# Performance work log

Hardware: AMD Instinct MI355X
Metric: run time of the kernel (lower is better)

The kernel has to match this reference:

```python
import jax, jax.numpy as jnp
import numpy as np

B, T, D = 1, 2048, 4096
N, K, H = 32, 8, 128  # num_heads, num_kv_heads, head_dim
ROPE_BASE = 10000
SCALE_FACTOR = 1.0
EPS = 1e-6
NEG_INF = -1e9


def rms_norm(x):
    var = jnp.mean(jnp.square(x), axis=-1, keepdims=True)
    return x * jax.lax.rsqrt(var + EPS)


def apply_rope(x, positions, base_frequency, scale_factor=1.0):
    # x: [B, L, num_heads, H], positions: [B, L]
    head_dim = x.shape[-1]
    fraction = 2.0 * jnp.arange(head_dim // 2, dtype=jnp.float32) / head_dim
    timescale = base_frequency ** fraction  # [H/2]
    sinusoid = positions[..., None].astype(jnp.float32) / timescale  # [B,L,H/2]
    sinusoid = sinusoid[..., None, :] / scale_factor  # [B,L,1,H/2]
    sin, cos = jnp.sin(sinusoid), jnp.cos(sinusoid)
    x1, x2 = jnp.split(x, 2, axis=-1)
    return jnp.concatenate([x1 * cos - x2 * sin, x2 * cos + x1 * sin], axis=-1)


def setup_inputs() -> dict:
    key = jax.random.key(0)
    ks = jax.random.split(key, 7)
    x = jax.random.normal(ks[0], (B, T, D), dtype=jnp.float32)
    segment_pos = jnp.broadcast_to(jnp.arange(T, dtype=jnp.int32)[None, :], (B, T))
    causal = jnp.tril(jnp.ones((T, T), dtype=bool))
    attn_mask = jnp.where(causal, 0.0, NEG_INF).astype(jnp.float32)[None]  # [B,T,S]
    attn_mask = jnp.broadcast_to(attn_mask, (B, T, T))
    q_w = jax.random.normal(ks[1], (N, D, H), dtype=jnp.float32) * (D ** -0.5)
    kv_w = jax.random.normal(ks[2], (2, K, D, H), dtype=jnp.float32) * (D ** -0.5)
    o_w = jax.random.normal(ks[3], (N, H, D), dtype=jnp.float32) * ((N * H) ** -0.5)
    q_scale = jax.random.normal(ks[4], (H,), dtype=jnp.float32) * 0.02  # RMSNorm scale (zeros-init style)
    k_scale = jax.random.normal(ks[5], (H,), dtype=jnp.float32) * 0.02
    return {"x": x, "segment_pos": segment_pos, "attn_mask": attn_mask,
            "q_w": q_w, "kv_w": kv_w, "o_w": o_w,
            "q_scale": q_scale, "k_scale": k_scale}


def reference(x, segment_pos, attn_mask, q_w, kv_w, o_w, q_scale, k_scale):
    # Projections
    q = jnp.einsum('BTD,NDH->BTNH', x, q_w)          # [B,T,N,H]
    kv = jnp.einsum('BSD,CKDH->CBSKH', x, kv_w)      # [2,B,S,K,H]
    k, v = kv[0], kv[1]
    # QK RMSNorm (with scale, (1+scale) convention) and value RMSNorm (no scale)
    q = rms_norm(q) * (1.0 + q_scale)
    k = rms_norm(k) * (1.0 + k_scale)
    v = rms_norm(v)
    # RoPE (standard path: positions are [B,L])
    q = apply_rope(q, segment_pos, ROPE_BASE, SCALE_FACTOR)
    k = apply_rope(k, segment_pos, ROPE_BASE, SCALE_FACTOR)
    # GQA grouping: [B,T,K,G,H]
    G = N // K
    qg = q.reshape(B, T, K, G, H)
    attn_logits = jnp.einsum('btkgh,bskh->bkgts', qg, k)  # [B,K,G,T,S]
    attn_logits = attn_logits + attn_mask[:, None, None, :, :]
    attn_weights = jax.nn.softmax(attn_logits, axis=-1).astype(v.dtype)
    out = jnp.einsum('bkgts,bskh->btkgh', attn_weights, v)  # [B,T,K,G,H]
    out = out.reshape(B, T, N, H)
    return jnp.einsum('BTNH,NHD->BTD', out, o_w)
```

## Files before the change

### kernel.cpp

```cpp
#include <hip/hip_runtime.h>
#include <stdint.h>


typedef __bf16 bf16x8 __attribute__((ext_vector_type(8)));
typedef float  f32x4  __attribute__((ext_vector_type(4)));

__device__ __forceinline__ uint16_t f2bf(float f) {
    union { float f; uint32_t u; } v; v.f = f;
    uint32_t r = v.u + 0x7fffu + ((v.u >> 16) & 1u);
    return (uint16_t)(r >> 16);
}

__device__ __forceinline__ void gload_lds16(const void* g, void* l) {
    __builtin_amdgcn_global_load_lds(
        (const __attribute__((address_space(1))) uint32_t*)g,
        (__attribute__((address_space(3))) uint32_t*)l, 16, 0, 0);
}

__global__ __launch_bounds__(256) void k_cvt_x(const float* __restrict__ x,
                                               uint16_t* __restrict__ xb) {
    int i = (blockIdx.x * 256 + threadIdx.x) * 8;
    int r = i >> 12, k = i & 4095;
    float4 a = *(const float4*)(x + i);
    float4 b = *(const float4*)(x + i + 4);
    uint16_t tmp[8];
    tmp[0] = f2bf(a.x); tmp[1] = f2bf(a.y); tmp[2] = f2bf(a.z); tmp[3] = f2bf(a.w);
    tmp[4] = f2bf(b.x); tmp[5] = f2bf(b.y); tmp[6] = f2bf(b.z); tmp[7] = f2bf(b.w);
    int dst = r * 4096 + (k & ~63) + (((((k >> 3) & 7) ^ (r & 7))) << 3);
    *(uint4*)(xb + dst) = *(uint4*)tmp;
}

__global__ __launch_bounds__(256) void k_prep_wt(const float* __restrict__ qw,
                                                 const float* __restrict__ kvw,
                                                 uint16_t* __restrict__ Wt) {
    const int hx = blockIdx.x, dx = blockIdx.y, m = blockIdx.z;
    const float* src = (m < 32) ? (qw + (size_t)m * 524288)
                                : (kvw + (size_t)(m - 32) * 524288);
    __shared__ uint16_t tile[64][65];
    const int t = threadIdx.x, d0 = dx * 64, h0 = hx * 64;
#pragma unroll
    for (int i = 0; i < 16; ++i) {
        int idx = i * 256 + t, r = idx >> 6, c = idx & 63;
        tile[r][c] = f2bf(src[(size_t)(d0 + r) * 128 + h0 + c]);
    }
    __syncthreads();
#pragma unroll
    for (int it = 0; it < 2; ++it) {
        int slot = it * 256 + t, hr = slot >> 3, cl = slot & 7;
        int R = m * 128 + h0 + hr;
        uint16_t tmp[8];
#pragma unroll
        for (int e = 0; e < 8; ++e) tmp[e] = tile[cl * 8 + e][hr];
        *(uint4*)&Wt[(size_t)R * 4096 + d0 + ((cl ^ (R & 7)) << 3)] = *(uint4*)tmp;
    }
}

__global__ __launch_bounds__(256) void k_prep_ot(const float* __restrict__ ow,
                                                 uint16_t* __restrict__ Ot) {
    const int dx = blockIdx.x, hx = blockIdx.y, n = blockIdx.z;
    const float* src = ow + (size_t)n * 524288;
    __shared__ uint16_t tile[64][65];
    const int t = threadIdx.x, h0 = hx * 64, d0 = dx * 64;
#pragma unroll
    for (int i = 0; i < 16; ++i) {
        int idx = i * 256 + t, r = idx >> 6, c = idx & 63;
        tile[r][c] = f2bf(src[(size_t)(h0 + r) * 4096 + d0 + c]);
    }
    __syncthreads();
#pragma unroll
    for (int it = 0; it < 2; ++it) {
        int slot = it * 256 + t, dr = slot >> 3, cl = slot & 7;
        int R = d0 + dr;
        uint16_t tmp[8];
#pragma unroll
        for (int e = 0; e < 8; ++e) tmp[e] = tile[cl * 8 + e][dr];
        *(uint4*)&Ot[(size_t)R * 4096 + n * 128 + h0 + ((cl ^ (R & 7)) << 3)] = *(uint4*)tmp;
    }
}

#define PH_BAR do { asm volatile("" ::: "memory"); \
                    __builtin_amdgcn_s_barrier(); \
                    asm volatile("" ::: "memory"); } while (0)
#define WAIT_LGKM do { asm volatile("s_waitcnt lgkmcnt(0)" ::: "memory"); \
                       __builtin_amdgcn_sched_barrier(0); } while (0)
#define WAIT_VM(N) do { asm volatile("s_waitcnt vmcnt(" #N ")" ::: "memory"); \
                        __builtin_amdgcn_sched_barrier(0); } while (0)

__global__ __launch_bounds__(512, 2) void k_gemm_qkv(const uint16_t* __restrict__ A,
                                                     const uint16_t* __restrict__ Bt,
                                                     const int* __restrict__ pos,
                                                     const float* __restrict__ qs,
                                                     const float* __restrict__ ks,
                                                     uint16_t* __restrict__ Qg,
                                                     uint16_t* __restrict__ Kg,
                                                     uint16_t* __restrict__ Vg) {
    extern __shared__ __align__(16) char smem[];
    uint16_t* lds = (uint16_t*)smem;
    const int Kd = 4096;
    const int t = threadIdx.x, wid = t >> 6, lane = t & 63;
    const int l16 = lane & 15, quad = lane >> 4;
    const int wr = wid >> 2, wc = wid & 3;
    const int bx = blockIdx.x, bm0 = blockIdx.y * 256, bn0 = bx * 256;

    f32x4 acc[8][4];
    const f32x4 z4 = {0.f, 0.f, 0.f, 0.f};
#pragma unroll
    for (int i = 0; i < 8; ++i)
#pragma unroll
        for (int j = 0; j < 4; ++j) acc[i][j] = z4;

    const int r0 = wid * 16 + (lane >> 2), c4 = lane & 3;
    const int sw2 = (r0 >> 1) & 3, sw7 = r0 & 7;
    const int offK0 = (((c4 ^ sw2)) ^ sw7) * 8;
    const int offK1 = ((4 + (c4 ^ sw2)) ^ sw7) * 8;
    const uint16_t* pA0 = A + (size_t)(bm0 + r0) * Kd;
    const uint16_t* pA1 = pA0 + (size_t)128 * Kd;
    const uint16_t* pB0 = Bt + (size_t)(bn0 + r0) * Kd;
    const uint16_t* pB1 = pB0 + (size_t)128 * Kd;
    uint16_t* stA = lds + wid * 512;
    uint16_t* stB = lds + 32768 + wid * 512;

    const int sA = (l16 >> 1) & 3;
    const int rdA = (wr * 128 + l16) * 32 + ((quad ^ sA) << 3);
    const int rdB = 32768 + (wc * 64 + l16) * 32 + ((quad ^ sA) << 3);

    bf16x8 af[4], bf[4];

#define STAGE_A(SLAB, OFF, TT) do { \
    gload_lds16(pA0 + (size_t)(TT) * 64 + (OFF), stA + (SLAB) * 8192); \
    gload_lds16(pA1 + (size_t)(TT) * 64 + (OFF), stA + (SLAB) * 8192 + 4096); } while (0)
#define STAGE_B(SLAB, OFF, TT) do { \
    gload_lds16(pB0 + (size_t)(TT) * 64 + (OFF), stB + (SLAB) * 8192); \
    gload_lds16(pB1 + (size_t)(TT) * 64 + (OFF), stB + (SLAB) * 8192 + 4096); } while (0)
#define LOAD_AF4(SLAB, I0) do { _Pragma("unroll") \
    for (int i_ = 0; i_ < 4; ++i_) \
        af[i_] = *(const bf16x8*)&lds[(SLAB) * 8192 + rdA + ((I0) + i_) * 512]; } while (0)
#define LOAD_BF4(SLAB) do { _Pragma("unroll") \
    for (int j_ = 0; j_ < 4; ++j_) \
        bf[j_] = *(const bf16x8*)&lds[(SLAB) * 8192 + rdB + j_ * 512]; } while (0)
#define MFMA_PH(I0) do { __builtin_amdgcn_s_setprio(1); \
    _Pragma("unroll") for (int i_ = 0; i_ < 4; ++i_) \
        _Pragma("unroll") for (int j_ = 0; j_ < 4; ++j_) \
            acc[(I0) + i_][j_] = __builtin_amdgcn_mfma_f32_16x16x32_bf16(af[i_], bf[j_], acc[(I0) + i_][j_], 0, 0, 0); \
    __builtin_amdgcn_s_setprio(0); } while (0)

#define TILE(TT, BUF) do { \
     \
    LOAD_BF4(2*(BUF)); LOAD_AF4(2*(BUF), 0); \
    STAGE_A((((BUF)^1)*2+1), offK1, (TT)+1); \
    PH_BAR; WAIT_LGKM; MFMA_PH(0); PH_BAR; \
     \
    LOAD_AF4(2*(BUF), 4); \
    WAIT_VM(6); \
    STAGE_B((((BUF)^1)*2+1), offK1, (TT)+1); \
    PH_BAR; WAIT_LGKM; MFMA_PH(4); PH_BAR; \
     \
    LOAD_BF4(2*(BUF)+1); LOAD_AF4(2*(BUF)+1, 0); \
    STAGE_A((BUF)*2, offK0, (TT)+2); \
    PH_BAR; WAIT_LGKM; MFMA_PH(0); PH_BAR; \
     \
    LOAD_AF4(2*(BUF)+1, 4); \
    WAIT_VM(6); \
    STAGE_B((BUF)*2, offK0, (TT)+2); \
    PH_BAR; WAIT_LGKM; MFMA_PH(4); PH_BAR; \
} while (0)

    STAGE_A(0, offK0, 0); STAGE_B(0, offK0, 0);
    STAGE_A(1, offK1, 0); STAGE_B(1, offK1, 0);
    STAGE_A(2, offK0, 1); STAGE_B(2, offK0, 1);
    WAIT_VM(8);
    PH_BAR;

#pragma unroll 1
    for (int Ti = 0; Ti < 31; ++Ti) {
        TILE(2 * Ti, 0);
        TILE(2 * Ti + 1, 1);
    }

    STAGE_A(3, offK1, 63); STAGE_B(3, offK1, 63);
    WAIT_VM(0);
    PH_BAR;
#pragma unroll
    for (int T = 62; T < 64; ++T) {
        const int BUF = T & 1;
        LOAD_BF4(2*BUF); LOAD_AF4(2*BUF, 0);     PH_BAR; WAIT_LGKM; MFMA_PH(0); PH_BAR;
        LOAD_AF4(2*BUF, 4);                      PH_BAR; WAIT_LGKM; MFMA_PH(4); PH_BAR;
        LOAD_BF4(2*BUF+1); LOAD_AF4(2*BUF+1, 0); PH_BAR; WAIT_LGKM; MFMA_PH(0); PH_BAR;
        LOAD_AF4(2*BUF+1, 4);                    PH_BAR; WAIT_LGKM; MFMA_PH(4); PH_BAR;
    }

#undef TILE
#undef MFMA_PH
#undef LOAD_BF4
#undef LOAD_AF4
#undef STAGE_B
#undef STAGE_A

    float* X   = (float*)smem;
    float* ssq = (float*)(smem + 133120);

#pragma unroll
    for (int i = 0; i < 8; ++i)
#pragma unroll
        for (int r = 0; r < 4; ++r) {
            float s = 0.f;
#pragma unroll
            for (int j = 0; j < 4; ++j) s += acc[i][j][r] * acc[i][j][r];
            s += __shfl_xor(s, 1); s += __shfl_xor(s, 2);
            s += __shfl_xor(s, 4); s += __shfl_xor(s, 8);
            if (l16 == 0)
                ssq[(wr * 128 + i * 16 + quad * 4 + r) * 4 + (wc >> 1) * 2 + (wc & 1)] = s;
        }
    __syncthreads();

    const int cat = (bx < 16) ? 0 : (bx < 20 ? 1 : 2);
    float s1 = 0.f, s2 = 0.f, invts = 0.f;
    if (cat < 2) {
        const float* sc = cat ? ks : qs;
        s1 = 1.0f + sc[lane];
        s2 = 1.0f + sc[lane + 64];
        invts = exp2f((float)lane * -0.20762050593046014f);
    }

#pragma unroll
    for (int pass = 0; pass < 2; ++pass) {
        if (wr == pass) {
#pragma unroll
            for (int i = 0; i < 8; ++i)
#pragma unroll
                for (int j = 0; j < 4; ++j)
#pragma unroll
                    for (int r = 0; r < 4; ++r)
                        X[(i * 16 + quad * 4 + r) * 260 + wc * 64 + j * 16 + l16] = acc[i][j][r];
        }
        __syncthreads();
        for (int rr = 0; rr < 16; ++rr) {
            const int lrow = wid * 16 + rr;
            const int grow = bm0 + pass * 128 + lrow;
            float sn = 0.f, cs = 0.f;
            if (cat < 2) {
                float ang = (float)pos[grow] * invts;
                __sincosf(ang, &sn, &cs);
            }
#pragma unroll
            for (int hh = 0; hh < 2; ++hh) {
                const int sb = (pass * 128 + lrow) * 4 + hh * 2;
                float rn = rsqrtf((ssq[sb] + ssq[sb + 1]) * 0.0078125f + 1e-6f);
                float x1 = X[lrow * 260 + hh * 128 + lane];
                float x2 = X[lrow * 260 + hh * 128 + 64 + lane];
                if (cat < 2) {
                    float y1 = x1 * rn * s1, y2 = x2 * rn * s2;
                    X[lrow * 260 + hh * 128 + lane]      = y1 * cs - y2 * sn;
                    X[lrow * 260 + hh * 128 + 64 + lane] = y2 * cs + y1 * sn;
                } else {
                    X[lrow * 260 + hh * 128 + lane]      = x1 * rn;
                    X[lrow * 260 + hh * 128 + 64 + lane] = x2 * rn;
                }
            }
        }
        __syncthreads();
        if (cat == 2) {
#pragma unroll
            for (int it = 0; it < 8; ++it) {
                int slot = it * 512 + t, hh = slot >> 11, rem = slot & 2047;
                int h = rem >> 4, sc2 = rem & 15;
                uint16_t tmp[8];
#pragma unroll
                for (int e = 0; e < 8; ++e)
                    tmp[e] = f2bf(X[(sc2 * 8 + e) * 260 + hh * 128 + h]);
                int n = bx * 2 + hh;
                *(uint4*)&Vg[((size_t)(n - 40) * 128 + h) * 2048 + (bm0 + pass * 128)
                             + ((sc2 ^ (h & 15)) << 3)] = *(uint4*)tmp;
            }
        } else {
#pragma unroll
            for (int it = 0; it < 8; ++it) {
                int slot = it * 512 + t, hh = slot >> 11, rem = slot & 2047;
                int lrow = rem >> 4, c = rem & 15;
                int tg = bm0 + pass * 128 + lrow, n = bx * 2 + hh;
                f32x4 a = *(f32x4*)&X[lrow * 260 + hh * 128 + c * 8];
                f32x4 b = *(f32x4*)&X[lrow * 260 + hh * 128 + c * 8 + 4];
                uint16_t tmp[8];
#pragma unroll
                for (int e = 0; e < 4; ++e) { tmp[e] = f2bf(a[e]); tmp[4 + e] = f2bf(b[e]); }
                if (cat == 0)
                    *(uint4*)&Qg[((size_t)n * 2048 + tg) * 128 + c * 8] = *(uint4*)tmp;
                else
                    *(uint4*)&Kg[((size_t)(n - 32) * 2048 + tg) * 128
                                 + ((c ^ (tg & 15)) << 3)] = *(uint4*)tmp;
            }
        }
        __syncthreads();
    }
}

__global__ __launch_bounds__(512, 2) void k_gemm2p(const uint16_t* __restrict__ A,
                                                   const uint16_t* __restrict__ Bt,
                                                   float* __restrict__ C) {
    extern __shared__ __align__(16) char smem2[];
    uint16_t* lds = (uint16_t*)smem2;
    const int Kd = 4096, Nn = 4096;
    const int t = threadIdx.x, wid = t >> 6, lane = t & 63;
    const int l16 = lane & 15, quad = lane >> 4;
    const int wr = wid >> 1, wc = wid & 1;
    const int bm0 = blockIdx.y * 256, bn0 = blockIdx.x * 128;

    f32x4 acc[4][4];
    const f32x4 z4 = {0.f, 0.f, 0.f, 0.f};
#pragma unroll
    for (int i = 0; i < 4; ++i)
#pragma unroll
        for (int j = 0; j < 4; ++j) acc[i][j] = z4;

    const int r0 = wid * 16 + (lane >> 2), c4 = lane & 3;
    const int sw2 = (r0 >> 1) & 3, sw7 = r0 & 7;
    const int offK0 = ((c4 ^ sw2) ^ sw7) * 8;
    const int offK1 = ((4 + (c4 ^ sw2)) ^ sw7) * 8;
    const uint16_t* pA0 = A + (size_t)(bm0 + r0) * Kd;
    const uint16_t* pA1 = pA0 + (size_t)128 * Kd;
    const uint16_t* pB0 = Bt + (size_t)(bn0 + r0) * Kd;
    uint16_t* stA = lds + wid * 512;
    uint16_t* stB = lds + 49152 + wid * 512;

    const int sA = (l16 >> 1) & 3;
    const int rdA = (wr * 64 + l16) * 32 + ((quad ^ sA) << 3);
    const int rdB = 49152 + (wc * 64 + l16) * 32 + ((quad ^ sA) << 3);

    bf16x8 af[4], bf[4];

#define G2_STAGE(SLAB, OFF, TT) do { \
    gload_lds16(pA0 + (size_t)(TT) * 64 + (OFF), stA + (SLAB) * 8192); \
    gload_lds16(pA1 + (size_t)(TT) * 64 + (OFF), stA + (SLAB) * 8192 + 4096); \
    gload_lds16(pB0 + (size_t)(TT) * 64 + (OFF), stB + (SLAB) * 4096); } while (0)

#define G2_MFMA do { __builtin_amdgcn_s_setprio(1); \
    _Pragma("unroll") for (int i_ = 0; i_ < 4; ++i_) \
        _Pragma("unroll") for (int j_ = 0; j_ < 4; ++j_) \
            acc[i_][j_] = __builtin_amdgcn_mfma_f32_16x16x32_bf16(af[i_], bf[j_], acc[i_][j_], 0, 0, 0); \
    __builtin_amdgcn_s_setprio(0); } while (0)

#define G2_LOAD(CS) do { _Pragma("unroll") \
    for (int i_ = 0; i_ < 4; ++i_) \
        af[i_] = *(const bf16x8*)&lds[(CS) * 8192 + rdA + i_ * 512]; \
    _Pragma("unroll") for (int j_ = 0; j_ < 4; ++j_) \
        bf[j_] = *(const bf16x8*)&lds[(CS) * 4096 + rdB + j_ * 512]; } while (0)

#define G2_PH(CS, SG, OFF, TT) do { \
    G2_LOAD(CS); \
    WAIT_VM(6); \
    G2_STAGE((SG), (OFF), (TT)); \
    PH_BAR; WAIT_LGKM; G2_MFMA; PH_BAR; } while (0)

#define G2_PHT(CS, VMN) do { \
    G2_LOAD(CS); \
    WAIT_VM(VMN); \
    PH_BAR; WAIT_LGKM; G2_MFMA; PH_BAR; } while (0)

    G2_STAGE(0, offK0, 0);
    G2_STAGE(1, offK1, 0);
    G2_STAGE(2, offK0, 1);
    G2_STAGE(3, offK1, 1);
    WAIT_VM(9);
    PH_BAR;

#pragma unroll 1
    for (int Tb = 0; Tb < 60; Tb += 3) {
        G2_PH(0, 4, offK0, Tb + 2);  G2_PH(1, 5, offK1, Tb + 2);
        G2_PH(2, 0, offK0, Tb + 3);  G2_PH(3, 1, offK1, Tb + 3);
        G2_PH(4, 2, offK0, Tb + 4);  G2_PH(5, 3, offK1, Tb + 4);
    }
    G2_PH(0, 4, offK0, 62);  G2_PH(1, 5, offK1, 62);
    G2_PH(2, 0, offK0, 63);  G2_PH(3, 1, offK1, 63);
    G2_PHT(4, 6); G2_PHT(5, 3); G2_PHT(0, 0); G2_PHT(1, 0);

#undef G2_PHT
#undef G2_PH
#undef G2_LOAD
#undef G2_MFMA
#undef G2_STAGE

#pragma unroll
    for (int i = 0; i < 4; ++i)
#pragma unroll
        for (int j = 0; j < 4; ++j) {
            int row = bm0 + wr * 64 + i * 16 + quad * 4;
            int col = bn0 + wc * 64 + j * 16 + l16;
            float* cp = C + (size_t)row * Nn + col;
            cp[0]              = acc[i][j][0];
            cp[(size_t)Nn]     = acc[i][j][1];
            cp[2 * (size_t)Nn] = acc[i][j][2];
            cp[3 * (size_t)Nn] = acc[i][j][3];
        }
}

__global__ __launch_bounds__(256) void k_attn(const uint16_t* __restrict__ Q,
                                              const uint16_t* __restrict__ K,
                                              const uint16_t* __restrict__ Vt,
                                              uint16_t* __restrict__ att) {
    __shared__ uint16_t sK[128 * 128];
    __shared__ uint16_t sV[128 * 128];
    const int p = blockIdx.x, n = blockIdx.y, kk = n >> 2;
    const int t = threadIdx.x, wave = t >> 6, lane = t & 63;
    const int l16 = lane & 15, quad = lane >> 4;
    const f32x4 z4 = {0.f, 0.f, 0.f, 0.f};

    const uint16_t* Kbase = K  + ((size_t)kk * 2048 + wave * 32 + (lane >> 4)) * 128 + (lane & 15) * 8;
    const uint16_t* Vbase = Vt + ((size_t)kk * 128  + wave * 32 + (lane >> 4)) * 2048 + (lane & 15) * 8;

    for (int half = 0; half < 2; ++half) {
        const int qt = half ? (31 - p) : p;
        const int q0 = qt * 64;
        const int nk = (qt >> 1) + 1;

        bf16x8 qf[4];
#pragma unroll
        for (int kc = 0; kc < 4; ++kc)
            qf[kc] = *(const bf16x8*)(Q + (size_t)(n * 2048 + q0 + wave * 16 + l16) * 128 + kc * 32 + quad * 8);

        f32x4 O[8];
#pragma unroll
        for (int h = 0; h < 8; ++h) O[h] = z4;
        float mrow[4], lrow[4];
#pragma unroll
        for (int r = 0; r < 4; ++r) { mrow[r] = -INFINITY; lrow[r] = 0.f; }

        for (int st = 0; st < nk; ++st) {
            const int s0 = st * 128;
            __syncthreads();
#pragma unroll
            for (int j = 0; j < 8; ++j) {
                gload_lds16(Kbase + (size_t)(s0 + j * 4) * 128, &sK[(wave * 32 + j * 4) * 128]);
                gload_lds16(Vbase + (size_t)j * 4 * 2048 + s0,  &sV[(wave * 32 + j * 4) * 128]);
            }
            __syncthreads();

            f32x4 S[8];
#pragma unroll
            for (int jn = 0; jn < 8; ++jn) S[jn] = z4;
#pragma unroll
            for (int jn = 0; jn < 8; ++jn) {
                int krow = jn * 16 + l16;
#pragma unroll
                for (int kc = 0; kc < 4; ++kc) {
                    bf16x8 b = *(const bf16x8*)&sK[krow * 128 + (((kc * 4 + quad) ^ l16) << 3)];
                    S[jn] = __builtin_amdgcn_mfma_f32_16x16x32_bf16(qf[kc], b, S[jn], 0, 0, 0);
                }
            }
            if (st == nk - 1) {
#pragma unroll
                for (int jn = 0; jn < 8; ++jn) {
                    int sc = s0 + jn * 16 + l16;
#pragma unroll
                    for (int r = 0; r < 4; ++r) {
                        int mr = q0 + wave * 16 + quad * 4 + r;
                        if (sc > mr) S[jn][r] = -INFINITY;
                    }
                }
            }
            float alpha[4];
#pragma unroll
            for (int r = 0; r < 4; ++r) {
                float mx = S[0][r];
#pragma unroll
                for (int jn = 1; jn < 8; ++jn) mx = fmaxf(mx, S[jn][r]);
                mx = fmaxf(mx, __shfl_xor(mx, 1));
                mx = fmaxf(mx, __shfl_xor(mx, 2));
                mx = fmaxf(mx, __shfl_xor(mx, 4));
                mx = fmaxf(mx, __shfl_xor(mx, 8));
                float mnew = fmaxf(mrow[r], mx);
                float a = __expf(mrow[r] - mnew);
                mrow[r] = mnew;
                float sum = 0.f;
#pragma unroll
                for (int jn = 0; jn < 8; ++jn) {
                    float e = __expf(S[jn][r] - mnew);
                    S[jn][r] = e;
                    sum += e;
                }
                sum += __shfl_xor(sum, 1);
                sum += __shfl_xor(sum, 2);
                sum += __shfl_xor(sum, 4);
                sum += __shfl_xor(sum, 8);
                lrow[r] = lrow[r] * a + sum;
                alpha[r] = a;
            }
#pragma unroll
            for (int h = 0; h < 8; ++h)
#pragma unroll
                for (int r = 0; r < 4; ++r) O[h][r] *= alpha[r];

            __syncthreads();
#pragma unroll
            for (int jn = 0; jn < 8; ++jn)
#pragma unroll
                for (int r = 0; r < 4; ++r) {
                    int prow = wave * 16 + quad * 4 + r;
                    int pcol = jn * 16 + l16;
                    sK[prow * 128 + ((pcol & 7) | ((((pcol >> 3) ^ prow) & 15) << 3))]
                        = f2bf(S[jn][r]);
                }
            bf16x8 pf[4];
#pragma unroll
            for (int ksv = 0; ksv < 4; ++ksv)
                pf[ksv] = *(const bf16x8*)&sK[(wave * 16 + l16) * 128 + (((ksv * 4 + quad) ^ l16) << 3)];
#pragma unroll
            for (int hj = 0; hj < 8; ++hj) {
                int vrow = hj * 16 + l16;
#pragma unroll
                for (int ksv = 0; ksv < 4; ++ksv) {
                    bf16x8 b = *(const bf16x8*)&sV[vrow * 128 + (((ksv * 4 + quad) ^ l16) << 3)];
                    O[hj] = __builtin_amdgcn_mfma_f32_16x16x32_bf16(pf[ksv], b, O[hj], 0, 0, 0);
                }
            }
        }

        __syncthreads();
        uint16_t* sO = &sK[wave * 2112];
        float inv[4];
#pragma unroll
        for (int r = 0; r < 4; ++r) inv[r] = 1.0f / lrow[r];
#pragma unroll
        for (int hj = 0; hj < 8; ++hj)
#pragma unroll
            for (int r = 0; r < 4; ++r)
                sO[(quad * 4 + r) * 132 + hj * 16 + l16] = f2bf(O[hj][r] * inv[r]);
#pragma unroll
        for (int it = 0; it < 4; ++it) {
            int slot = it * 64 + lane, rloc = slot >> 4, cl = slot & 15;
            bf16x8 v = *(const bf16x8*)&sO[rloc * 132 + cl * 8];
            int R = q0 + wave * 16 + rloc;
            size_t dst = (size_t)R * 4096 + n * 128 + ((cl & 8) << 3) + (((cl & 7) ^ (R & 7)) << 3);
            *(uint4*)&att[dst] = *(uint4*)&v;
        }
    }
}

extern "C" void kernel_launch(void* const* d_in, const int* in_sizes, int n_in,
                              void* d_out, int out_size, void* d_ws, size_t ws_size,
                              hipStream_t stream) {
    const float* x   = (const float*)d_in[0];
    const int*   sp  = (const int*)d_in[1];
    const float* qw  = (const float*)d_in[3];
    const float* kvw = (const float*)d_in[4];
    const float* ow  = (const float*)d_in[5];
    const float* qsc = (const float*)d_in[6];
    const float* ksc = (const float*)d_in[7];
    float* out = (float*)d_out;

    char* ws = (char*)d_ws;
    uint16_t* xb   = (uint16_t*)(ws);
    uint16_t* Wt   = (uint16_t*)(ws + (size_t)(16u << 20));
    uint16_t* Qb   = (uint16_t*)(ws + (size_t)(64u << 20));
    uint16_t* Kb   = (uint16_t*)(ws + (size_t)(80u << 20));
    uint16_t* Vtb  = (uint16_t*)(ws + (size_t)(84u << 20));
    uint16_t* att  = (uint16_t*)(ws);
    uint16_t* Ot   = (uint16_t*)(ws + (size_t)(16u << 20));

    static bool attr_done = false;
    if (!attr_done) {
        hipFuncSetAttribute(reinterpret_cast<const void*>(k_gemm_qkv),
                            hipFuncAttributeMaxDynamicSharedMemorySize, 137216);
        hipFuncSetAttribute(reinterpret_cast<const void*>(k_gemm2p),
                            hipFuncAttributeMaxDynamicSharedMemorySize, 147456);
        attr_done = true;
    }

    k_cvt_x    <<<4096, 256, 0, stream>>>(x, xb);
    k_prep_wt  <<<dim3(2, 64, 48), 256, 0, stream>>>(qw, kvw, Wt);
    k_gemm_qkv <<<dim3(24, 8), 512, 137216, stream>>>(xb, Wt, sp, qsc, ksc, Qb, Kb, Vtb);
    k_prep_ot  <<<dim3(64, 2, 32), 256, 0, stream>>>(ow, Ot);
    k_attn     <<<dim3(16, 32), 256, 0, stream>>>(Qb, Kb, Vtb, att);
    k_gemm2p   <<<dim3(32, 8), 512, 147456, stream>>>(att, Ot, out);
}
```

Baseline: 530.6 us.

## Double-buffer MFMA operand registers to overlap LDS reads with MFMA in both GEMMs

Both GEMM main loops now keep two sets of A/B fragment registers. LDS reads for the next phase are issued while the MFMAs of the current phase run. The explicit lgkmcnt(0) wait and one of the two barriers per phase are removed, and the vmcnt thresholds and epilogues are adjusted to match. This is meant to hide LDS read latency behind matrix math, at the cost of more VGPRs and more delicate synchronisation correctness.

```diff
diff --git a/kernel.cpp b/kernel.cpp
--- a/kernel.cpp
+++ b/kernel.cpp
@@ -81,10 +81,9 @@
 #define PH_BAR do { asm volatile("" ::: "memory"); \
                     __builtin_amdgcn_s_barrier(); \
                     asm volatile("" ::: "memory"); } while (0)
-#define WAIT_LGKM do { asm volatile("s_waitcnt lgkmcnt(0)" ::: "memory"); \
-                       __builtin_amdgcn_sched_barrier(0); } while (0)
 #define WAIT_VM(N) do { asm volatile("s_waitcnt vmcnt(" #N ")" ::: "memory"); \
                         __builtin_amdgcn_sched_barrier(0); } while (0)
+#define SCHED0 __builtin_amdgcn_sched_barrier(0)
 
 __global__ __launch_bounds__(512, 2) void k_gemm_qkv(const uint16_t* __restrict__ A,
                                                      const uint16_t* __restrict__ Bt,
@@ -124,7 +123,7 @@
     const int rdA = (wr * 128 + l16) * 32 + ((quad ^ sA) << 3);
     const int rdB = 32768 + (wc * 64 + l16) * 32 + ((quad ^ sA) << 3);
 
-    bf16x8 af[4], bf[4];
+    bf16x8 afA[4], afB[4], bfA[4], bfB[4];
 
 #define STAGE_A(SLAB, OFF, TT) do { \
     gload_lds16(pA0 + (size_t)(TT) * 64 + (OFF), stA + (SLAB) * 8192); \
@@ -132,37 +131,33 @@
 #define STAGE_B(SLAB, OFF, TT) do { \
     gload_lds16(pB0 + (size_t)(TT) * 64 + (OFF), stB + (SLAB) * 8192); \
     gload_lds16(pB1 + (size_t)(TT) * 64 + (OFF), stB + (SLAB) * 8192 + 4096); } while (0)
-#define LOAD_AF4(SLAB, I0) do { _Pragma("unroll") \
+#define RD_A(DST, SLAB, I0) do { _Pragma("unroll") \
     for (int i_ = 0; i_ < 4; ++i_) \
-        af[i_] = *(const bf16x8*)&lds[(SLAB) * 8192 + rdA + ((I0) + i_) * 512]; } while (0)
-#define LOAD_BF4(SLAB) do { _Pragma("unroll") \
+        DST[i_] = *(const bf16x8*)&lds[(SLAB) * 8192 + rdA + ((I0) + i_) * 512]; } while (0)
+#define RD_B(DST, SLAB) do { _Pragma("unroll") \
     for (int j_ = 0; j_ < 4; ++j_) \
-        bf[j_] = *(const bf16x8*)&lds[(SLAB) * 8192 + rdB + j_ * 512]; } while (0)
-#define MFMA_PH(I0) do { __builtin_amdgcn_s_setprio(1); \
+        DST[j_] = *(const bf16x8*)&lds[(SLAB) * 8192 + rdB + j_ * 512]; } while (0)
+#define MFMA16(AF, BF, I0) do { __builtin_amdgcn_s_setprio(1); \
     _Pragma("unroll") for (int i_ = 0; i_ < 4; ++i_) \
         _Pragma("unroll") for (int j_ = 0; j_ < 4; ++j_) \
-            acc[(I0) + i_][j_] = __builtin_amdgcn_mfma_f32_16x16x32_bf16(af[i_], bf[j_], acc[(I0) + i_][j_], 0, 0, 0); \
+            acc[(I0) + i_][j_] = __builtin_amdgcn_mfma_f32_16x16x32_bf16(AF[i_], BF[j_], acc[(I0) + i_][j_], 0, 0, 0); \
     __builtin_amdgcn_s_setprio(0); } while (0)
 
 #define TILE(TT, BUF) do { \
-     \
-    LOAD_BF4(2*(BUF)); LOAD_AF4(2*(BUF), 0); \
-    STAGE_A((((BUF)^1)*2+1), offK1, (TT)+1); \
-    PH_BAR; WAIT_LGKM; MFMA_PH(0); PH_BAR; \
-     \
-    LOAD_AF4(2*(BUF), 4); \
-    WAIT_VM(6); \
-    STAGE_B((((BUF)^1)*2+1), offK1, (TT)+1); \
-    PH_BAR; WAIT_LGKM; MFMA_PH(4); PH_BAR; \
-     \
-    LOAD_BF4(2*(BUF)+1); LOAD_AF4(2*(BUF)+1, 0); \
-    STAGE_A((BUF)*2, offK0, (TT)+2); \
-    PH_BAR; WAIT_LGKM; MFMA_PH(0); PH_BAR; \
-     \
-    LOAD_AF4(2*(BUF)+1, 4); \
-    WAIT_VM(6); \
-    STAGE_B((BUF)*2, offK0, (TT)+2); \
-    PH_BAR; WAIT_LGKM; MFMA_PH(4); PH_BAR; \
+    RD_A(afB, 2*(BUF), 4); \
+    WAIT_VM(4); \
+    STAGE_A(2*((BUF)^1)+1, offK1, (TT)+1); \
+    SCHED0; MFMA16(afA, bfA, 0); PH_BAR; \
+    RD_A(afA, 2*(BUF)+1, 0); RD_B(bfB, 2*(BUF)+1); \
+    STAGE_B(2*((BUF)^1)+1, offK1, (TT)+1); \
+    SCHED0; MFMA16(afB, bfA, 4); PH_BAR; \
+    RD_A(afB, 2*(BUF)+1, 4); \
+    WAIT_VM(4); \
+    STAGE_A(2*(BUF), offK0, (TT)+2); \
+    SCHED0; MFMA16(afA, bfB, 0); PH_BAR; \
+    RD_A(afA, 2*((BUF)^1), 0); RD_B(bfA, 2*((BUF)^1)); \
+    STAGE_B(2*(BUF), offK0, (TT)+2); \
+    SCHED0; MFMA16(afB, bfB, 4); PH_BAR; \
 } while (0)
 
     STAGE_A(0, offK0, 0); STAGE_B(0, offK0, 0);
@@ -170,6 +165,7 @@
     STAGE_A(2, offK0, 1); STAGE_B(2, offK0, 1);
     WAIT_VM(8);
     PH_BAR;
+    RD_A(afA, 0, 0); RD_B(bfA, 0);
 
 #pragma unroll 1
     for (int Ti = 0; Ti < 31; ++Ti) {
@@ -177,22 +173,26 @@
         TILE(2 * Ti + 1, 1);
     }
 
-    STAGE_A(3, offK1, 63); STAGE_B(3, offK1, 63);
-    WAIT_VM(0);
-    PH_BAR;
-#pragma unroll
-    for (int T = 62; T < 64; ++T) {
-        const int BUF = T & 1;
-        LOAD_BF4(2*BUF); LOAD_AF4(2*BUF, 0);     PH_BAR; WAIT_LGKM; MFMA_PH(0); PH_BAR;
-        LOAD_AF4(2*BUF, 4);                      PH_BAR; WAIT_LGKM; MFMA_PH(4); PH_BAR;
-        LOAD_BF4(2*BUF+1); LOAD_AF4(2*BUF+1, 0); PH_BAR; WAIT_LGKM; MFMA_PH(0); PH_BAR;
-        LOAD_AF4(2*BUF+1, 4);                    PH_BAR; WAIT_LGKM; MFMA_PH(4); PH_BAR;
-    }
+    RD_A(afB, 0, 4); WAIT_VM(4); STAGE_A(3, offK1, 63);
+    SCHED0; MFMA16(afA, bfA, 0); PH_BAR;
+    RD_A(afA, 1, 0); RD_B(bfB, 1); STAGE_B(3, offK1, 63);
+    SCHED0; MFMA16(afB, bfA, 4); PH_BAR;
+    RD_A(afB, 1, 4); WAIT_VM(4);
+    SCHED0; MFMA16(afA, bfB, 0); PH_BAR;
+    RD_A(afA, 2, 0); RD_B(bfA, 2);
+    SCHED0; MFMA16(afB, bfB, 4); PH_BAR;
+    RD_A(afB, 2, 4); WAIT_VM(0);
+    SCHED0; MFMA16(afA, bfA, 0); PH_BAR;
+    RD_A(afA, 3, 0); RD_B(bfB, 3);
+    SCHED0; MFMA16(afB, bfA, 4); PH_BAR;
+    RD_A(afB, 3, 4);
+    SCHED0; MFMA16(afA, bfB, 0); PH_BAR;
+    SCHED0; MFMA16(afB, bfB, 4);
 
 #undef TILE
-#undef MFMA_PH
-#undef LOAD_BF4
-#undef LOAD_AF4
+#undef MFMA16
+#undef RD_B
+#undef RD_A
 #undef STAGE_B
 #undef STAGE_A
 
@@ -326,57 +326,58 @@
     const int rdA = (wr * 64 + l16) * 32 + ((quad ^ sA) << 3);
     const int rdB = 49152 + (wc * 64 + l16) * 32 + ((quad ^ sA) << 3);
 
-    bf16x8 af[4], bf[4];
+    bf16x8 afA[4], afB[4], bfA[4], bfB[4];
 
 #define G2_STAGE(SLAB, OFF, TT) do { \
     gload_lds16(pA0 + (size_t)(TT) * 64 + (OFF), stA + (SLAB) * 8192); \
     gload_lds16(pA1 + (size_t)(TT) * 64 + (OFF), stA + (SLAB) * 8192 + 4096); \
     gload_lds16(pB0 + (size_t)(TT) * 64 + (OFF), stB + (SLAB) * 4096); } while (0)
-
-#define G2_MFMA do { __builtin_amdgcn_s_setprio(1); \
+#define G2_RD(AD, BD, CS) do { _Pragma("unroll") \
+    for (int i_ = 0; i_ < 4; ++i_) \
+        AD[i_] = *(const bf16x8*)&lds[(CS) * 8192 + rdA + i_ * 512]; \
+    _Pragma("unroll") for (int j_ = 0; j_ < 4; ++j_) \
+        BD[j_] = *(const bf16x8*)&lds[(CS) * 4096 + rdB + j_ * 512]; } while (0)
+#define G2_MFMA(AF, BF) do { __builtin_amdgcn_s_setprio(1); \
     _Pragma("unroll") for (int i_ = 0; i_ < 4; ++i_) \
         _Pragma("unroll") for (int j_ = 0; j_ < 4; ++j_) \
-            acc[i_][j_] = __builtin_amdgcn_mfma_f32_16x16x32_bf16(af[i_], bf[j_], acc[i_][j_], 0, 0, 0); \
+            acc[i_][j_] = __builtin_amdgcn_mfma_f32_16x16x32_bf16(AF[i_], BF[j_], acc[i_][j_], 0, 0, 0); \
     __builtin_amdgcn_s_setprio(0); } while (0)
 
-#define G2_LOAD(CS) do { _Pragma("unroll") \
-    for (int i_ = 0; i_ < 4; ++i_) \
-        af[i_] = *(const bf16x8*)&lds[(CS) * 8192 + rdA + i_ * 512]; \
-    _Pragma("unroll") for (int j_ = 0; j_ < 4; ++j_) \
-        bf[j_] = *(const bf16x8*)&lds[(CS) * 4096 + rdB + j_ * 512]; } while (0)
-
-#define G2_PH(CS, SG, OFF, TT) do { \
-    G2_LOAD(CS); \
-    WAIT_VM(6); \
-    G2_STAGE((SG), (OFF), (TT)); \
-    PH_BAR; WAIT_LGKM; G2_MFMA; PH_BAR; } while (0)
-
-#define G2_PHT(CS, VMN) do { \
-    G2_LOAD(CS); \
-    WAIT_VM(VMN); \
-    PH_BAR; WAIT_LGKM; G2_MFMA; PH_BAR; } while (0)
+#define G2_PH(RA, RB, CSN, SST, OFF, TT, MA, MB) do { \
+    G2_RD(RA, RB, CSN); \
+    WAIT_VM(3); \
+    G2_STAGE(SST, OFF, TT); \
+    SCHED0; G2_MFMA(MA, MB); PH_BAR; } while (0)
 
     G2_STAGE(0, offK0, 0);
     G2_STAGE(1, offK1, 0);
     G2_STAGE(2, offK0, 1);
     G2_STAGE(3, offK1, 1);
-    WAIT_VM(9);
+    WAIT_VM(6);
     PH_BAR;
+    G2_RD(afA, bfA, 0);
 
 #pragma unroll 1
-    for (int Tb = 0; Tb < 60; Tb += 3) {
-        G2_PH(0, 4, offK0, Tb + 2);  G2_PH(1, 5, offK1, Tb + 2);
-        G2_PH(2, 0, offK0, Tb + 3);  G2_PH(3, 1, offK1, Tb + 3);
-        G2_PH(4, 2, offK0, Tb + 4);  G2_PH(5, 3, offK1, Tb + 4);
-    }
-    G2_PH(0, 4, offK0, 62);  G2_PH(1, 5, offK1, 62);
-    G2_PH(2, 0, offK0, 63);  G2_PH(3, 1, offK1, 63);
-    G2_PHT(4, 6); G2_PHT(5, 3); G2_PHT(0, 0); G2_PHT(1, 0);
-
-#undef G2_PHT
+    for (int m = 0; m < 20; ++m) {
+        G2_PH(afB, bfB, 1, 4, offK0, 3*m + 2, afA, bfA);
+        G2_PH(afA, bfA, 2, 5, offK1, 3*m + 2, afB, bfB);
+        G2_PH(afB, bfB, 3, 0, offK0, 3*m + 3, afA, bfA);
+        G2_PH(afA, bfA, 4, 1, offK1, 3*m + 3, afB, bfB);
+        G2_PH(afB, bfB, 5, 2, offK0, 3*m + 4, afA, bfA);
+        G2_PH(afA, bfA, 0, 3, offK1, 3*m + 4, afB, bfB);
+    }
+    G2_PH(afB, bfB, 1, 4, offK0, 62, afA, bfA);
+    G2_PH(afA, bfA, 2, 5, offK1, 62, afB, bfB);
+    G2_PH(afB, bfB, 3, 0, offK0, 63, afA, bfA);
+    G2_PH(afA, bfA, 4, 1, offK1, 63, afB, bfB);
+    G2_RD(afB, bfB, 5); WAIT_VM(3); SCHED0; G2_MFMA(afA, bfA); PH_BAR;
+    G2_RD(afA, bfA, 0); WAIT_VM(0); SCHED0; G2_MFMA(afB, bfB); PH_BAR;
+    G2_RD(afB, bfB, 1);              SCHED0; G2_MFMA(afA, bfA); PH_BAR;
+    SCHED0; G2_MFMA(afB, bfB);
+
 #undef G2_PH
-#undef G2_LOAD
 #undef G2_MFMA
+#undef G2_RD
 #undef G2_STAGE
 
 #pragma unroll
```

Result: faster. 514.4 us (-3.1%).
